# Optimization experiments

Measured on AMD Instinct MI355X. Metric: run time of the kernel, lower is better.

## Reference

```python
import jax, jax.numpy as jnp
import numpy as np

SIMPLE_W = 1.0
NON_SIMPLE_W = 5.0

# connectivity offset sets (exclude center)
_ALL26 = [(a, b, c) for a in (-1, 0, 1) for b in (-1, 0, 1) for c in (-1, 0, 1) if (a, b, c) != (0, 0, 0)]
OFF6 = [o for o in _ALL26 if abs(o[0]) + abs(o[1]) + abs(o[2]) == 1]          # scipy default structure
OFF18 = [o for o in _ALL26 if not (abs(o[0]) == 1 and abs(o[1]) == 1 and abs(o[2]) == 1)]  # the 's' structure
OFF26 = _ALL26                                                                  # np.ones((3,3,3))


def global_label(fg):
    """Connected-component labels (6-connectivity) via max-propagation.
    Labels are distinct positive ints per component (values differ from scipy's
    1..K but only label *equality* is used downstream). fg: bool [D,H,W]."""
    D, H, W = fg.shape
    idx = (jnp.arange(fg.size, dtype=jnp.int32) + 1).reshape(fg.shape)
    lab0 = jnp.where(fg, idx, 0)

    def step(lab):
        p = jnp.pad(lab, 1)
        m = lab
        for dz, dy, dx in OFF6:
            m = jnp.maximum(m, p[1 + dz:1 + dz + D, 1 + dy:1 + dy + H, 1 + dx:1 + dx + W])
        return jnp.where(fg, m, 0)

    def cond(c):
        return ~c[1]

    def body(c):
        lab, _ = c
        new = step(lab)
        return new, jnp.all(new == lab)

    lab, _ = jax.lax.while_loop(cond, body, (lab0, jnp.array(False)))
    return lab


def local_ncomp(mask, offsets):
    """Number of connected components inside each 3x3x3 window.
    mask: bool [N,3,3,3]. Max-propagation of unique seeds for 26 iters
    (>= max path length among 27 voxels); a component is counted where the
    surviving max label equals its own seed."""
    seed = (jnp.arange(27, dtype=jnp.int32) + 1).reshape(3, 3, 3)
    lab0 = jnp.where(mask, seed, 0)

    def body(_, lab):
        p = jnp.pad(lab, ((0, 0), (1, 1), (1, 1), (1, 1)))
        m = lab
        for dz, dy, dx in offsets:
            m = jnp.maximum(m, p[:, 1 + dz:4 + dz, 1 + dy:4 + dy, 1 + dx:4 + dx])
        return jnp.where(mask, m, 0)

    lab = jax.lax.fori_loop(0, 26, body, lab0)
    return jnp.sum((lab == seed) & mask, axis=(1, 2, 3))


def nonsimple_map(x):
    """Per-voxel non-simple-point indicator, float, same shape as x."""
    D, H, W = x.shape
    fg = x > 0
    glab = global_label(fg)
    p = jnp.pad(glab, 1, mode='edge')  # np.pad(..., 'edge')
    # 3x3x3 label windows per voxel -> [N,3,3,3]
    wins = jnp.stack([p[dz:dz + D, dy:dy + H, dx:dx + W]
                      for dz in range(3) for dy in range(3) for dx in range(3)], axis=-1)
    wins = wins.reshape(-1, 3, 3, 3)
    center = wins[:, 1, 1, 1]  # [N]
    c = center[:, None, None, None]
    # test 1: complement-of-center-label components (18-connectivity) must be exactly 1
    n1 = local_ncomp(wins != c, OFF18)
    # test 2: center-label components with center voxel removed (26-conn) must be exactly 1
    mask2 = (wins == c).at[:, 1, 1, 1].set(False)
    n2 = local_ncomp(mask2, OFF26)
    ns = (center != 0) & ((n1 != 1) | (n2 != 1))
    return ns.reshape(D, H, W).astype(x.dtype)


def setup_inputs() -> dict:
    key = jax.random.key(0)
    k1, k2 = jax.random.split(key)
    D = H = W = 64
    prediction = jax.random.normal(k1, (D, H, W), dtype=jnp.float32)
    label = jax.random.randint(k2, (D, H, W), 0, 2).astype(jnp.float32)
    return {"prediction": prediction, "label": label}


def reference(prediction, label):
    pw = nonsimple_map(prediction)
    lw = nonsimple_map(label)
    w_bool = (pw + lw) > 0
    weight = jnp.where(w_bool, NON_SIMPLE_W, SIMPLE_W).astype(prediction.dtype)
    # BCEWithLogitsLoss(reduction='none'): max(x,0) - x*y + log(1+exp(-|x|))
    cost = jnp.maximum(prediction, 0.0) - prediction * label + jnp.log1p(jnp.exp(-jnp.abs(prediction)))
    return jnp.mean(weight * cost)
```

## Files before the change

kernel.cpp:

```cpp
#include <hip/hip_runtime.h>

#define DIM 64
#define NVOX (DIM * DIM * DIM)
#define EPF 53248

__device__ __forceinline__ void unite(int* L, int a, int b) {
    int ra = a, rb = b;
    while (ra != rb) {
        if (ra > rb) { int t = ra; ra = rb; rb = t; }
        int old = atomicMin(&L[rb], ra);
        if (old == rb || old == ra) break;
        rb = old;
    }
}

__device__ __forceinline__ int chase(const int* __restrict__ L, int p) {
    int q = L[p];
    while (q != p) { p = q; q = L[p]; }
    return p;
}

__global__ __launch_bounds__(512)
void local_ccl(const float* __restrict__ pred,
               const float* __restrict__ lab,
               int* __restrict__ LP, int* __restrict__ LL,
               float* __restrict__ out) {
    __shared__ int s_lab[2048];
    int t = threadIdx.x;
    if (blockIdx.x == 0 && blockIdx.y == 0 && t == 0) *out = 0.0f;
    int b = blockIdx.x;
    int tx = b & 3, ty = (b >> 2) & 3, tz = b >> 4;
    int X0 = tx << 4, Y0 = ty << 4, Z0 = tz << 3;

    const float* src = blockIdx.y ? lab : pred;
    int* Lg = blockIdx.y ? LL : LP;

    int l0 = t << 2;
    int v0 = ((Z0 + (l0 >> 8)) << 12) | ((Y0 + ((l0 >> 4) & 15)) << 6)
           | (X0 + (l0 & 15));

    unsigned nib;
    {
        const float4 f = *reinterpret_cast<const float4*>(src + v0);
        nib  = (unsigned)(f.x > 0.0f);
        nib |= (unsigned)(f.y > 0.0f) << 1;
        nib |= (unsigned)(f.z > 0.0f) << 2;
        nib |= (unsigned)(f.w > 0.0f) << 3;
    }

    unsigned rm = nib << ((t & 3) << 2);
    rm |= __shfl_xor(rm, 1, 64);
    rm |= __shfl_xor(rm, 2, 64);

    int rowbase = l0 & ~15;
    int xbase = l0 & 15;

    {
        int4 s;
        int lbl[4];
#pragma unroll
        for (int k = 0; k < 4; ++k) {
            int xpos = xbase + k;
            unsigned u = ~rm & ((1u << xpos) - 1u);
            int start = u ? (32 - __clz(u)) : 0;
            lbl[k] = ((nib >> k) & 1) ? rowbase + start : -1;
        }
        s.x = lbl[0]; s.y = lbl[1]; s.z = lbl[2]; s.w = lbl[3];
        *reinterpret_cast<int4*>(&s_lab[l0]) = s;
    }
    __syncthreads();

    {
        int py_a = -2, py_b = -2;
        int pz_a = -2, pz_b = -2;
#pragma unroll
        for (int k = 0; k < 4; ++k) {
            if (!((nib >> k) & 1)) continue;
            int l = l0 + k;
            int a = s_lab[l0 + k] >= 0 ? (l0 + k, s_lab[l]) : -1;
            a = s_lab[l];
            int ly = (l >> 4) & 15, lz = l >> 8;
            if (ly < 15) {
                int nb = s_lab[l + 16];
                if (nb >= 0 && !(a == py_a && nb == py_b)) {
                    unite(s_lab, a, nb);
                    py_a = a; py_b = nb;
                }
            }
            if (lz < 7) {
                int nb = s_lab[l + 256];
                if (nb >= 0 && !(a == pz_a && nb == pz_b)) {
                    unite(s_lab, a, nb);
                    pz_a = a; pz_b = nb;
                }
            }
        }
    }
    __syncthreads();

    {
        int rr[4];
#pragma unroll
        for (int k = 0; k < 4; ++k) {
            int g = -1;
            if ((nib >> k) & 1) {
                int p = s_lab[l0 + k];
                while (s_lab[p] != p) p = s_lab[p];
                g = ((Z0 + (p >> 8)) << 12) | ((Y0 + ((p >> 4) & 15)) << 6)
                  | (X0 + (p & 15));
            }
            rr[k] = g;
        }
        *reinterpret_cast<int4*>(Lg + v0) = make_int4(rr[0], rr[1], rr[2], rr[3]);
    }
}

__global__ __launch_bounds__(256)
void boundary_link(int* __restrict__ LP, int* __restrict__ LL) {
    int r = blockIdx.x * blockDim.x + threadIdx.x;
    int* L = blockIdx.y ? LL : LP;

    int v, n;
    if (r < 12288) {
        int plane = 15 + ((r >> 12) << 4);
        int ij = r & 4095;
        v = ((ij >> 6) << 12) | ((ij & 63) << 6) | plane;
        n = v + 1;
    } else if (r < 24576) {
        int r2 = r - 12288;
        int plane = 15 + ((r2 >> 12) << 4);
        int ij = r2 & 4095;
        v = ((ij >> 6) << 12) | (plane << 6) | (ij & 63);
        n = v + 64;
    } else {
        int r3 = r - 24576;
        int plane = 7 + ((r3 >> 12) << 3);
        int ij = r3 & 4095;
        v = (plane << 12) | ((ij >> 6) << 6) | (ij & 63);
        n = v + 4096;
    }

    int lane = threadIdx.x & 63;

    int pa = L[v], pb = L[n];
    bool go = (pa >= 0) & (pb >= 0);

    int xpa = __shfl_up(pa, 1, 64), xpb = __shfl_up(pb, 1, 64);
    if (lane && xpa == pa && xpb == pb) go = false;

    int r0 = -1, r1 = -1;
    if (go) {
        int u0 = chase(L, pa), u1 = chase(L, pb);
        r0 = min(u0, u1); r1 = max(u0, u1);
    }

    int q0 = __shfl_up(r0, 1, 64), q1 = __shfl_up(r1, 1, 64);
    bool dup = lane && (q0 == r0) && (q1 == r1);

    if (r0 >= 0 && r0 != r1 && !dup) unite(L, r0, r1);
}

#define MX_L 0x6DB6DB6u
#define MX_R 0x36DB6DBu
#define MY_L 0x7E3F1F8u
#define MY_R 0x0FC7E3Fu
#define M27  0x7FFFFFFu

__device__ __forceinline__ unsigned dil26(unsigned m) {
    m |= ((m << 1) & MX_L) | ((m >> 1) & MX_R);
    m |= ((m << 3) & MY_L) | ((m >> 3) & MY_R);
    m |= ((m << 9) & M27)  | (m >> 9);
    return m;
}
__device__ __forceinline__ unsigned dil18(unsigned m) {
    unsigned ax = m | ((m << 1) & MX_L) | ((m >> 1) & MX_R);
    unsigned ay = m | ((m << 3) & MY_L) | ((m >> 3) & MY_R);
    unsigned dxy = ax | ((ax << 3) & MY_L) | ((ax >> 3) & MY_R);
    unsigned dxz = ax | ((ax << 9) & M27)  | (ax >> 9);
    unsigned dyz = ay | ((ay << 9) & M27)  | (ay >> 9);
    return dxy | dxz | dyz;
}

__device__ __forceinline__ bool single18(unsigned m) {
    if (!m) return false;
    unsigned c = m & (~m + 1u);
    for (;;) {
        unsigned n = dil18(c) & m;
        if (n == m) return true;
        if (n == c) return false;
        c = n;
    }
}
__device__ __forceinline__ bool single26(unsigned m) {
    if (!m) return false;
    unsigned c = m & (~m + 1u);
    for (;;) {
        unsigned n = dil26(c) & m;
        if (n == m) return true;
        if (n == c) return false;
        c = n;
    }
}

#define HV2 600

__global__ __launch_bounds__(256, 4)
void finalize_kernel(const float* __restrict__ pred,
                     const float* __restrict__ lab,
                     const int* __restrict__ LP,
                     const int* __restrict__ LL,
                     float* __restrict__ out) {
    __shared__ int sP[HV2], sL[HV2];
    __shared__ float s_part[4];
    int t = threadIdx.x;
    int b = blockIdx.x;
    int rx = b & 7, ry = (b >> 3) & 7, rz = b >> 6;
    int x0 = rx << 3, y0 = ry << 3, z0 = rz << 2;

    int pv[3], lv[3];
#pragma unroll
    for (int j = 0; j < 3; ++j) {
        int i = t + (j << 8);
        if (i < HV2) {
            int hx = i % 10, rr = i / 10, hy = rr % 10, hz = rr / 10;
            int gx = x0 + hx - 1; gx = gx < 0 ? 0 : (gx > 63 ? 63 : gx);
            int gy = y0 + hy - 1; gy = gy < 0 ? 0 : (gy > 63 ? 63 : gy);
            int gz = z0 + hz - 1; gz = gz < 0 ? 0 : (gz > 63 ? 63 : gz);
            int gv = (gz << 12) | (gy << 6) | gx;
            pv[j] = LP[gv];
            lv[j] = LL[gv];
        }
    }
#pragma unroll
    for (int j = 0; j < 3; ++j) {
        int i = t + (j << 8);
        if (i < HV2) {
            int p = pv[j];
            if (p >= 0) p = chase(LP, p);
            sP[i] = p;
            p = lv[j];
            if (p >= 0) p = chase(LL, p);
            sL[i] = p;
        }
    }
    __syncthreads();

    float acc;
    {
        int l = t;
        int lx = l & 7, ly = (l >> 3) & 7, lz = l >> 6;
        int x = x0 | lx, y = y0 | ly, z = z0 | lz;
        int v = (z << 12) | (y << 6) | x;
        int base = lz * 100 + ly * 10 + lx;

        bool nsP = false, nsL = false;
        {
            int c = sP[base + 111];
            if (c >= 0) {
                unsigned m1 = 0, m2 = 0; int k = 0;
#pragma unroll
                for (int kz = 0; kz < 3; ++kz)
#pragma unroll
                    for (int ky = 0; ky < 3; ++ky)
#pragma unroll
                        for (int kx = 0; kx < 3; ++kx, ++k) {
                            int w = sP[base + kz * 100 + ky * 10 + kx];
                            m1 |= (unsigned)(w != c) << k;
                            m2 |= (unsigned)(w == c) << k;
                        }
                m2 &= ~(1u << 13);
                nsP = !(single18(m1) && single26(m2));
            }
        }
        {
            int c = sL[base + 111];
            if (c >= 0) {
                unsigned m1 = 0, m2 = 0; int k = 0;
#pragma unroll
                for (int kz = 0; kz < 3; ++kz)
#pragma unroll
                    for (int ky = 0; ky < 3; ++ky)
#pragma unroll
                        for (int kx = 0; kx < 3; ++kx, ++k) {
                            int w = sL[base + kz * 100 + ky * 10 + kx];
                            m1 |= (unsigned)(w != c) << k;
                            m2 |= (unsigned)(w == c) << k;
                        }
                m2 &= ~(1u << 13);
                nsL = !(single18(m1) && single26(m2));
            }
        }

        float p = pred[v], lvf = lab[v];
        float cost = fmaxf(p, 0.0f) - p * lvf + log1pf(__expf(-fabsf(p)));
        acc = ((nsP || nsL) ? 5.0f : 1.0f) * cost;
    }

#pragma unroll
    for (int off = 32; off > 0; off >>= 1)
        acc += __shfl_down(acc, off, 64);
    if ((t & 63) == 0) s_part[t >> 6] = acc;
    __syncthreads();
    if (t == 0) {
        float s = s_part[0] + s_part[1] + s_part[2] + s_part[3];
        atomicAdd(out, s * (1.0f / (float)NVOX));
    }
}

extern "C" void kernel_launch(void* const* d_in, const int* in_sizes, int n_in,
                              void* d_out, int out_size, void* d_ws, size_t ws_size,
                              hipStream_t stream) {
    const float* pred = (const float*)d_in[0];
    const float* lab  = (const float*)d_in[1];
    float* out = (float*)d_out;

    int* LP = (int*)d_ws;
    int* LL = LP + NVOX;

    hipLaunchKernelGGL(local_ccl, dim3(128, 2), dim3(512), 0, stream,
                       pred, lab, LP, LL, out);
    hipLaunchKernelGGL(boundary_link, dim3(EPF / 256, 2), dim3(256), 0, stream,
                       LP, LL);
    hipLaunchKernelGGL(finalize_kernel, dim3(1024), dim3(256), 0, stream,
                       pred, lab, LP, LL, out);
}
```

Before: 103.3 us.

## Replace tiled shared-memory CCL with global row-run seeding and run linking

Drops the two-phase labelling (per-tile union-find in shared memory followed by tile-boundary linking) in favour of seeding full 64-voxel x-runs in global memory and then uniting vertically and depth-adjacent runs directly with global atomics. This removes the shared-memory phase, the block syncs and the per-tile path chasing. In exchange every y and z adjacency now goes through global atomicMin union operations, which can add contention and longer union-find chains for the finalize kernel to resolve.

```diff
diff --git a/kernel.cpp b/kernel.cpp
--- a/kernel.cpp
+++ b/kernel.cpp
@@ -2,7 +2,6 @@
 
 #define DIM 64
 #define NVOX (DIM * DIM * DIM)
-#define EPF 53248
 
 __device__ __forceinline__ void unite(int* L, int a, int b) {
     int ra = a, rb = b;
@@ -20,24 +19,16 @@
     return p;
 }
 
-__global__ __launch_bounds__(512)
-void local_ccl(const float* __restrict__ pred,
-               const float* __restrict__ lab,
+__global__ __launch_bounds__(256)
+void seed_runs(const float* __restrict__ pred, const float* __restrict__ lab,
                int* __restrict__ LP, int* __restrict__ LL,
                float* __restrict__ out) {
-    __shared__ int s_lab[2048];
-    int t = threadIdx.x;
-    if (blockIdx.x == 0 && blockIdx.y == 0 && t == 0) *out = 0.0f;
-    int b = blockIdx.x;
-    int tx = b & 3, ty = (b >> 2) & 3, tz = b >> 4;
-    int X0 = tx << 4, Y0 = ty << 4, Z0 = tz << 3;
+    int tix = blockIdx.x * 256 + threadIdx.x;
+    if (blockIdx.x == 0 && blockIdx.y == 0 && threadIdx.x == 0) *out = 0.0f;
+    int v0 = tix << 2;
 
     const float* src = blockIdx.y ? lab : pred;
-    int* Lg = blockIdx.y ? LL : LP;
-
-    int l0 = t << 2;
-    int v0 = ((Z0 + (l0 >> 8)) << 12) | ((Y0 + ((l0 >> 4) & 15)) << 6)
-           | (X0 + (l0 & 15));
+    int* L = blockIdx.y ? LL : LP;
 
     unsigned nib;
     {
@@ -48,116 +39,51 @@
         nib |= (unsigned)(f.w > 0.0f) << 3;
     }
 
-    unsigned rm = nib << ((t & 3) << 2);
+    int seg = threadIdx.x & 15;
+    unsigned long long rm = (unsigned long long)nib << (seg << 2);
     rm |= __shfl_xor(rm, 1, 64);
     rm |= __shfl_xor(rm, 2, 64);
-
-    int rowbase = l0 & ~15;
-    int xbase = l0 & 15;
-
-    {
-        int4 s;
-        int lbl[4];
-#pragma unroll
-        for (int k = 0; k < 4; ++k) {
-            int xpos = xbase + k;
-            unsigned u = ~rm & ((1u << xpos) - 1u);
-            int start = u ? (32 - __clz(u)) : 0;
-            lbl[k] = ((nib >> k) & 1) ? rowbase + start : -1;
-        }
-        s.x = lbl[0]; s.y = lbl[1]; s.z = lbl[2]; s.w = lbl[3];
-        *reinterpret_cast<int4*>(&s_lab[l0]) = s;
-    }
-    __syncthreads();
-
-    {
-        int py_a = -2, py_b = -2;
-        int pz_a = -2, pz_b = -2;
-#pragma unroll
-        for (int k = 0; k < 4; ++k) {
-            if (!((nib >> k) & 1)) continue;
-            int l = l0 + k;
-            int a = s_lab[l0 + k] >= 0 ? (l0 + k, s_lab[l]) : -1;
-            a = s_lab[l];
-            int ly = (l >> 4) & 15, lz = l >> 8;
-            if (ly < 15) {
-                int nb = s_lab[l + 16];
-                if (nb >= 0 && !(a == py_a && nb == py_b)) {
-                    unite(s_lab, a, nb);
-                    py_a = a; py_b = nb;
-                }
-            }
-            if (lz < 7) {
-                int nb = s_lab[l + 256];
-                if (nb >= 0 && !(a == pz_a && nb == pz_b)) {
-                    unite(s_lab, a, nb);
-                    pz_a = a; pz_b = nb;
-                }
-            }
-        }
-    }
-    __syncthreads();
-
-    {
-        int rr[4];
-#pragma unroll
-        for (int k = 0; k < 4; ++k) {
-            int g = -1;
-            if ((nib >> k) & 1) {
-                int p = s_lab[l0 + k];
-                while (s_lab[p] != p) p = s_lab[p];
-                g = ((Z0 + (p >> 8)) << 12) | ((Y0 + ((p >> 4) & 15)) << 6)
-                  | (X0 + (p & 15));
-            }
-            rr[k] = g;
-        }
-        *reinterpret_cast<int4*>(Lg + v0) = make_int4(rr[0], rr[1], rr[2], rr[3]);
-    }
+    rm |= __shfl_xor(rm, 4, 64);
+    rm |= __shfl_xor(rm, 8, 64);
+
+    int rowstart = v0 & ~63;
+    int xb = seg << 2;
+
+    int lbl[4];
+#pragma unroll
+    for (int k = 0; k < 4; ++k) {
+        int x = xb + k;
+        unsigned long long u = ~rm & ((1ull << x) - 1ull);
+        int start = u ? (64 - __clzll(u)) : 0;
+        lbl[k] = ((nib >> k) & 1) ? rowstart + start : -1;
+    }
+    *reinterpret_cast<int4*>(L + v0) = make_int4(lbl[0], lbl[1], lbl[2], lbl[3]);
 }
 
 __global__ __launch_bounds__(256)
-void boundary_link(int* __restrict__ LP, int* __restrict__ LL) {
-    int r = blockIdx.x * blockDim.x + threadIdx.x;
+void link_runs(int* __restrict__ LP, int* __restrict__ LL) {
+    int tix = blockIdx.x * 256 + threadIdx.x;
+    int v0 = tix << 2;
     int* L = blockIdx.y ? LL : LP;
-
-    int v, n;
-    if (r < 12288) {
-        int plane = 15 + ((r >> 12) << 4);
-        int ij = r & 4095;
-        v = ((ij >> 6) << 12) | ((ij & 63) << 6) | plane;
-        n = v + 1;
-    } else if (r < 24576) {
-        int r2 = r - 12288;
-        int plane = 15 + ((r2 >> 12) << 4);
-        int ij = r2 & 4095;
-        v = ((ij >> 6) << 12) | (plane << 6) | (ij & 63);
-        n = v + 64;
-    } else {
-        int r3 = r - 24576;
-        int plane = 7 + ((r3 >> 12) << 3);
-        int ij = r3 & 4095;
-        v = (plane << 12) | ((ij >> 6) << 6) | (ij & 63);
-        n = v + 4096;
-    }
-
-    int lane = threadIdx.x & 63;
-
-    int pa = L[v], pb = L[n];
-    bool go = (pa >= 0) & (pb >= 0);
-
-    int xpa = __shfl_up(pa, 1, 64), xpb = __shfl_up(pb, 1, 64);
-    if (lane && xpa == pa && xpb == pb) go = false;
-
-    int r0 = -1, r1 = -1;
-    if (go) {
-        int u0 = chase(L, pa), u1 = chase(L, pb);
-        r0 = min(u0, u1); r1 = max(u0, u1);
-    }
-
-    int q0 = __shfl_up(r0, 1, 64), q1 = __shfl_up(r1, 1, 64);
-    bool dup = lane && (q0 == r0) && (q1 == r1);
-
-    if (r0 >= 0 && r0 != r1 && !dup) unite(L, r0, r1);
+    int dir = blockIdx.z;
+
+    int y = (v0 >> 6) & 63, z = v0 >> 12;
+    if (dir ? (z == 63) : (y == 63)) return;
+    int off = dir ? 4096 : 64;
+
+    const int4 a4 = *reinterpret_cast<const int4*>(L + v0);
+    const int4 b4 = *reinterpret_cast<const int4*>(L + v0 + off);
+    int a[4] = { a4.x, a4.y, a4.z, a4.w };
+    int b[4] = { b4.x, b4.y, b4.z, b4.w };
+
+    int pa = -2, pb = -2;
+#pragma unroll
+    for (int k = 0; k < 4; ++k) {
+        if (a[k] < 0 || b[k] < 0) continue;
+        if (a[k] == pa && b[k] == pb) continue;
+        unite(L, a[k], b[k]);
+        pa = a[k]; pb = b[k];
+    }
 }
 
 #define MX_L 0x6DB6DB6u
@@ -317,9 +243,9 @@
     int* LP = (int*)d_ws;
     int* LL = LP + NVOX;
 
-    hipLaunchKernelGGL(local_ccl, dim3(128, 2), dim3(512), 0, stream,
+    hipLaunchKernelGGL(seed_runs, dim3(NVOX / 1024, 2), dim3(256), 0, stream,
                        pred, lab, LP, LL, out);
-    hipLaunchKernelGGL(boundary_link, dim3(EPF / 256, 2), dim3(256), 0, stream,
+    hipLaunchKernelGGL(link_runs, dim3(NVOX / 1024, 2, 2), dim3(256), 0, stream,
                        LP, LL);
     hipLaunchKernelGGL(finalize_kernel, dim3(1024), dim3(256), 0, stream,
                        pred, lab, LP, LL, out);
```

New measurement: 337.4 us. 227% more time.

## Use path-compressing CAS union-find for global merge and interleave label halos

Applied to the files above, without the earlier changes.

The global boundary-merge kernel now does root finding with path halving and unites roots with atomicCAS instead of an atomicMin chain. This is meant to shorten later find chains and cut redundant atomics. The finalize kernel stores the prediction and label roots as an int2 array so one shared load serves both neighbourhood tests. It also derives the center-equal mask from the complement mask rather than building it separately. Path halving adds non-atomic writes to the label array, which is safe here only because parent pointers are monotone.

```diff
diff --git a/kernel.cpp b/kernel.cpp
--- a/kernel.cpp
+++ b/kernel.cpp
@@ -4,7 +4,30 @@
 #define NVOX (DIM * DIM * DIM)
 #define EPF 53248
 
-__device__ __forceinline__ void unite(int* L, int a, int b) {
+__device__ __forceinline__ int find_root_link(int* L, int v) {
+    for (;;) {
+        int p = L[v];
+        if (p == v) return v;
+        int gp = L[p];
+        if (gp == p) return p;
+        L[v] = gp;
+        v = gp;
+    }
+}
+
+__device__ __forceinline__ void unite_cas(int* L, int a, int b) {
+    int ra = find_root_link(L, a);
+    int rb = find_root_link(L, b);
+    while (ra != rb) {
+        if (ra > rb) { int t = ra; ra = rb; rb = t; }
+        int old = atomicCAS(&L[rb], rb, ra);
+        if (old == rb) break;
+        rb = find_root_link(L, old);
+        ra = find_root_link(L, ra);
+    }
+}
+
+__device__ __forceinline__ void unite_min(int* L, int a, int b) {
     int ra = a, rb = b;
     while (ra != rb) {
         if (ra > rb) { int t = ra; ra = rb; rb = t; }
@@ -77,20 +100,19 @@
         for (int k = 0; k < 4; ++k) {
             if (!((nib >> k) & 1)) continue;
             int l = l0 + k;
-            int a = s_lab[l0 + k] >= 0 ? (l0 + k, s_lab[l]) : -1;
-            a = s_lab[l];
+            int a = s_lab[l];
             int ly = (l >> 4) & 15, lz = l >> 8;
             if (ly < 15) {
                 int nb = s_lab[l + 16];
                 if (nb >= 0 && !(a == py_a && nb == py_b)) {
-                    unite(s_lab, a, nb);
+                    unite_min(s_lab, a, nb);
                     py_a = a; py_b = nb;
                 }
             }
             if (lz < 7) {
                 int nb = s_lab[l + 256];
                 if (nb >= 0 && !(a == pz_a && nb == pz_b)) {
-                    unite(s_lab, a, nb);
+                    unite_min(s_lab, a, nb);
                     pz_a = a; pz_b = nb;
                 }
             }
@@ -150,14 +172,14 @@
 
     int r0 = -1, r1 = -1;
     if (go) {
-        int u0 = chase(L, pa), u1 = chase(L, pb);
+        int u0 = find_root_link(L, pa), u1 = find_root_link(L, pb);
         r0 = min(u0, u1); r1 = max(u0, u1);
     }
 
     int q0 = __shfl_up(r0, 1, 64), q1 = __shfl_up(r1, 1, 64);
     bool dup = lane && (q0 == r0) && (q1 == r1);
 
-    if (r0 >= 0 && r0 != r1 && !dup) unite(L, r0, r1);
+    if (r0 >= 0 && r0 != r1 && !dup) unite_cas(L, r0, r1);
 }
 
 #define MX_L 0x6DB6DB6u
@@ -210,7 +232,7 @@
                      const int* __restrict__ LP,
                      const int* __restrict__ LL,
                      float* __restrict__ out) {
-    __shared__ int sP[HV2], sL[HV2];
+    __shared__ int2 sPL[HV2];
     __shared__ float s_part[4];
     int t = threadIdx.x;
     int b = blockIdx.x;
@@ -237,10 +259,9 @@
         if (i < HV2) {
             int p = pv[j];
             if (p >= 0) p = chase(LP, p);
-            sP[i] = p;
-            p = lv[j];
-            if (p >= 0) p = chase(LL, p);
-            sL[i] = p;
+            int l = lv[j];
+            if (l >= 0) l = chase(LL, l);
+            sPL[i] = make_int2(p, l);
         }
     }
     __syncthreads();
@@ -253,42 +274,28 @@
         int v = (z << 12) | (y << 6) | x;
         int base = lz * 100 + ly * 10 + lx;
 
+        const int2 c2 = sPL[base + 111];
+        unsigned m1P = 0, m1L = 0;
+        int k = 0;
+#pragma unroll
+        for (int kz = 0; kz < 3; ++kz)
+#pragma unroll
+            for (int ky = 0; ky < 3; ++ky)
+#pragma unroll
+                for (int kx = 0; kx < 3; ++kx, ++k) {
+                    const int2 w2 = sPL[base + kz * 100 + ky * 10 + kx];
+                    m1P |= (unsigned)(w2.x != c2.x) << k;
+                    m1L |= (unsigned)(w2.y != c2.y) << k;
+                }
+
         bool nsP = false, nsL = false;
-        {
-            int c = sP[base + 111];
-            if (c >= 0) {
-                unsigned m1 = 0, m2 = 0; int k = 0;
-#pragma unroll
-                for (int kz = 0; kz < 3; ++kz)
-#pragma unroll
-                    for (int ky = 0; ky < 3; ++ky)
-#pragma unroll
-                        for (int kx = 0; kx < 3; ++kx, ++k) {
-                            int w = sP[base + kz * 100 + ky * 10 + kx];
-                            m1 |= (unsigned)(w != c) << k;
-                            m2 |= (unsigned)(w == c) << k;
-                        }
-                m2 &= ~(1u << 13);
-                nsP = !(single18(m1) && single26(m2));
-            }
-        }
-        {
-            int c = sL[base + 111];
-            if (c >= 0) {
-                unsigned m1 = 0, m2 = 0; int k = 0;
-#pragma unroll
-                for (int kz = 0; kz < 3; ++kz)
-#pragma unroll
-                    for (int ky = 0; ky < 3; ++ky)
-#pragma unroll
-                        for (int kx = 0; kx < 3; ++kx, ++k) {
-                            int w = sL[base + kz * 100 + ky * 10 + kx];
-                            m1 |= (unsigned)(w != c) << k;
-                            m2 |= (unsigned)(w == c) << k;
-                        }
-                m2 &= ~(1u << 13);
-                nsL = !(single18(m1) && single26(m2));
-            }
+        if (c2.x >= 0) {
+            unsigned m2 = ~m1P & (M27 & ~(1u << 13));
+            nsP = !(single18(m1P) && single26(m2));
+        }
+        if (c2.y >= 0) {
+            unsigned m2 = ~m1L & (M27 & ~(1u << 13));
+            nsL = !(single18(m1L) && single26(m2));
         }
 
         float p = pred[v], lvf = lab[v];
```

After: 107.1 us. 1.04x slower.
